# Optimization experiments

Measured on AMD Instinct MI355X. Metric: run time of the kernel, lower is better.

## Reference

```python
import jax, jax.numpy as jnp
import numpy as np

D = 128          # kg_emb_dim
H = 8            # mha_n_heads
N = 20000        # sub-graph nodes per modality
NNZ = 500000     # incidence entries per modality
E = 5000         # hyperedges per modality
C = 50           # context entities
NENT = 50000     # n_entity (rec vocab)


def hyperconv(x, theta, bias, nodes, edges, num_edges):
    # PyG-style HypergraphConv: out = D^-1 H B^-1 H^T (X Theta) + b
    xt = x @ theta                                             # [N, D]
    ones = jnp.ones(nodes.shape[0], xt.dtype)
    e_sum = jax.ops.segment_sum(xt[nodes], edges, num_segments=num_edges)   # [E, D]
    e_deg = jax.ops.segment_sum(ones, edges, num_segments=num_edges)        # [E]
    m = e_sum / jnp.maximum(e_deg, 1.0)[:, None]               # hyperedge means
    n_sum = jax.ops.segment_sum(m[edges], nodes, num_segments=x.shape[0])   # [N, D]
    n_deg = jax.ops.segment_sum(ones, nodes, num_segments=x.shape[0])       # [N]
    return n_sum / jnp.maximum(n_deg, 1.0)[:, None] + bias


def mha(q_x, kv_x, Wq, bq, Wk, bk, Wv, bv, Wo, bo):
    # torch.nn.MultiheadAttention math, batch of 1 (squeezed)
    dh = D // H
    q = (q_x @ Wq + bq).reshape(-1, H, dh)
    k = (kv_x @ Wk + bk).reshape(-1, H, dh)
    v = (kv_x @ Wv + bv).reshape(-1, H, dh)
    scores = jnp.einsum('qhd,khd->hqk', q, k) / jnp.sqrt(jnp.asarray(dh, q.dtype))
    attn = jax.nn.softmax(scores, axis=-1)
    out = jnp.einsum('hqk,khd->qhd', attn, v).reshape(-1, D)
    return out @ Wo + bo


def self_attn(h, a, b):
    # SelfAttentionBatch: softmax(tanh(h a) b) weighted sum over rows
    e = (jnp.tanh(h @ a) @ b)[:, 0]
    return jax.nn.softmax(e) @ h


def setup_inputs() -> dict:
    ks = jax.random.split(jax.random.key(0), 32)
    s = D ** (-0.5)
    inp = {
        'item_emb':   jax.random.normal(ks[0], (N, D), jnp.float32) * s,
        'entity_emb': jax.random.normal(ks[1], (N, D), jnp.float32) * s,
        'word_emb':   jax.random.normal(ks[2], (N, D), jnp.float32) * s,
        'context_entity': jax.random.normal(ks[3], (C, D), jnp.float32) * s,
        'theta_item':   jax.random.normal(ks[4], (D, D), jnp.float32) * s,
        'bias_item':    jax.random.normal(ks[5], (D,), jnp.float32) * 0.02,
        'theta_entity': jax.random.normal(ks[6], (D, D), jnp.float32) * s,
        'bias_entity':  jax.random.normal(ks[7], (D,), jnp.float32) * 0.02,
        'theta_word':   jax.random.normal(ks[8], (D, D), jnp.float32) * s,
        'bias_word':    jax.random.normal(ks[9], (D,), jnp.float32) * 0.02,
        'Wq': jax.random.normal(ks[10], (D, D), jnp.float32) * s,
        'bq': jax.random.normal(ks[11], (D,), jnp.float32) * 0.02,
        'Wk': jax.random.normal(ks[12], (D, D), jnp.float32) * s,
        'bk': jax.random.normal(ks[13], (D,), jnp.float32) * 0.02,
        'Wv': jax.random.normal(ks[14], (D, D), jnp.float32) * s,
        'bv': jax.random.normal(ks[15], (D,), jnp.float32) * 0.02,
        'Wo': jax.random.normal(ks[16], (D, D), jnp.float32) * s,
        'bo': jax.random.normal(ks[17], (D,), jnp.float32) * 0.02,
        'a_his': jax.random.normal(ks[18], (D, D), jnp.float32) * s,
        'b_his': jax.random.normal(ks[19], (D, 1), jnp.float32) * s,
        'a_kg':  jax.random.normal(ks[20], (D, D), jnp.float32) * s,
        'b_kg':  jax.random.normal(ks[21], (D, 1), jnp.float32) * s,
        'rec_W': jax.random.normal(ks[22], (D, NENT), jnp.float32) * s,
        'rec_b': jax.random.normal(ks[23], (NENT,), jnp.float32) * 0.02,
        'item_nodes':   jax.random.randint(ks[24], (NNZ,), 0, N, jnp.int32),
        'item_edges':   jax.random.randint(ks[25], (NNZ,), 0, E, jnp.int32),
        'entity_nodes': jax.random.randint(ks[26], (NNZ,), 0, N, jnp.int32),
        'entity_edges': jax.random.randint(ks[27], (NNZ,), 0, E, jnp.int32),
        'word_nodes':   jax.random.randint(ks[28], (NNZ,), 0, N, jnp.int32),
        'word_edges':   jax.random.randint(ks[29], (NNZ,), 0, E, jnp.int32),
    }
    return inp


def reference(item_emb, entity_emb, word_emb, context_entity,
              theta_item, bias_item, theta_entity, bias_entity, theta_word, bias_word,
              Wq, bq, Wk, bk, Wv, bv, Wo, bo,
              a_his, b_his, a_kg, b_kg, rec_W, rec_b,
              item_nodes, item_edges, entity_nodes, entity_edges, word_nodes, word_edges):
    ih = hyperconv(item_emb, theta_item, bias_item, item_nodes, item_edges, E)
    eh = hyperconv(entity_emb, theta_entity, bias_entity, entity_nodes, entity_edges, E)
    wh = hyperconv(word_emb, theta_word, bias_word, word_nodes, word_edges, E)
    related = jnp.concatenate([ih, eh, wh], axis=0)            # [3N, D]
    # MHItemAttention: context queries attend over related embeddings
    attentive = mha(context_entity, related, Wq, bq, Wk, bk, Wv, bv, Wo, bo)  # [C, D]
    u = self_attn(attentive, a_his, b_his)                     # [D]
    user = jnp.concatenate([context_entity, u[None]], axis=0)  # [C+1, D]
    user_repr = self_attn(user, a_kg, b_kg)                    # [D]
    scores = user_repr @ rec_W + rec_b                         # [NENT]
    return scores
```

## Files before the change

### kernel.cpp

```cpp
#include <hip/hip_runtime.h>
#include <hip/hip_bf16.h>

#define D_ 128
#define H_ 8
#define N_ 20000
#define NNZ_ 500000
#define E_ 5000
#define C_ 50
#define NENT_ 50000
#define NK_ (3*N_)
#define CAPE_ 192
#define CAPN_ 64
#define ENT_PB 4096
#define NBKT 157
#define BCAP 3648
#define ABLK 123
#define NCH3 118
#define KVBLK 235
#define BINA_B (3*ABLK)
#define NBB (3*NBKT)
#define EGB 3752

struct Ptr3f { const float* p[3]; };
struct Ptr3i { const int* p[3]; };
struct GemmB { const float* A[3]; const float* W[3]; unsigned short* C[3]; };

typedef short bf16x8 __attribute__((ext_vector_type(8)));
typedef float f32x4  __attribute__((ext_vector_type(4)));
typedef float f32x2  __attribute__((ext_vector_type(2)));

__device__ __forceinline__ unsigned short f2b(float f){
  unsigned u = __float_as_uint(f);
  u += 0x7FFFu + ((u>>16)&1u);
  return (unsigned short)(u>>16);
}
__device__ __forceinline__ unsigned pk2(float a, float b){
  return (unsigned)f2b(a) | ((unsigned)f2b(b) << 16);
}
__device__ __forceinline__ float blo(unsigned u){ return __uint_as_float(u<<16); }
__device__ __forceinline__ float bhi(unsigned u){ return __uint_as_float(u & 0xFFFF0000u); }

#define GBATCH(SRC, SREG, LBASE) { \
  uint4 uu[8]; \
  _Pragma("unroll") \
  for (int kk=0;kk<8;kk++){ \
    int idx = __shfl(SREG, (LBASE) + 4*kk + rgrp); \
    uu[kk] = *(const uint4*)((SRC) + (size_t)idx*128 + dl*8); \
  } \
  _Pragma("unroll") \
  for (int kk=0;kk<8;kk++){ \
    a01 += (f32x2){blo(uu[kk].x), bhi(uu[kk].x)}; \
    a23 += (f32x2){blo(uu[kk].y), bhi(uu[kk].y)}; \
    a45 += (f32x2){blo(uu[kk].z), bhi(uu[kk].z)}; \
    a67 += (f32x2){blo(uu[kk].w), bhi(uu[kk].w)}; \
  } }

#define PB_PACK 7500
#define PB_Z    7628
#define PB_Q    7629
#define PB_CTX  7693
#define PB_TOT  7743
__global__ __launch_bounds__(256) void prep_binA(Ptr3f xs, unsigned short* __restrict__ xb,
    const float* __restrict__ Wk, const float* __restrict__ Wv, unsigned short* __restrict__ bfB,
    unsigned short* __restrict__ mzero,
    const float* __restrict__ ctx, const float* __restrict__ Wq, const float* __restrict__ bq,
    unsigned short* __restrict__ bfQ,
    const float* __restrict__ a2, const float* __restrict__ b2, float* __restrict__ e2,
    Ptr3i nodes, Ptr3i edges,
    unsigned* __restrict__ pe_part, unsigned* __restrict__ pn_part,
    int* __restrict__ gcnt_e, int* __restrict__ gcnt_n)
{
  const int t = threadIdx.x;
  if (blockIdx.x < BINA_B){
    __shared__ unsigned lbin[ENT_PB];
    __shared__ int cnt[256], off[256];
    __shared__ int gbase[NBKT];
    __shared__ int wsum[4];
    const int mod = blockIdx.x / ABLK;
    const int xblk = blockIdx.x - mod*ABLK;
    const int* nd = nodes.p[mod];
    const int* ed = edges.p[mod];
    const int base = xblk * ENT_PB;
    const int lane = t & 63, w = t >> 6;

    int myn[16], mye[16], pos[16];
    #pragma unroll
    for (int k=0;k<16;k++){
      int i = base + t + k*256;
      if (i < NNZ_){ myn[k]=nd[i]; mye[k]=ed[i]; }
      else { myn[k]=-1; mye[k]=-1; }
    }

    cnt[t] = 0;
    __syncthreads();
    #pragma unroll
    for (int k=0;k<16;k++)
      if (mye[k] >= 0) pos[k] = atomicAdd(&cnt[mye[k]>>5], 1);
    __syncthreads();
    {
      int v = cnt[t], s = v;
      #pragma unroll
      for (int d=1; d<64; d<<=1){ int u=__shfl_up(s,d); if (lane>=d) s+=u; }
      if (lane==63) wsum[w]=s;
      __syncthreads();
      int wb=0;
      for (int i=0;i<w;i++) wb+=wsum[i];
      off[t] = wb + s - v;
      __syncthreads();
    }
    #pragma unroll
    for (int k=0;k<16;k++)
      if (mye[k] >= 0)
        lbin[off[mye[k]>>5] + pos[k]] = ((unsigned)mye[k] << 15) | (unsigned)myn[k];
    if (t < NBKT && cnt[t] > 0) gbase[t] = atomicAdd(&gcnt_e[mod*NBKT + t], cnt[t]);
    __syncthreads();
    {
      int total = off[255];
      unsigned* dstreg = pe_part + (size_t)mod*NBKT*BCAP;
      for (int i=t; i<total; i+=256){
        unsigned pk = lbin[i];
        int b = pk >> 20;
        int gp = gbase[b] + (i - off[b]);
        if (gp < BCAP) dstreg[(size_t)b*BCAP + gp] = pk;
      }
    }
    __syncthreads();

    cnt[t] = 0;
    __syncthreads();
    #pragma unroll
    for (int k=0;k<16;k++)
      if (myn[k] >= 0) pos[k] = atomicAdd(&cnt[myn[k]>>7], 1);
    __syncthreads();
    {
      int v = cnt[t], s = v;
      #pragma unroll
      for (int d=1; d<64; d<<=1){ int u=__shfl_up(s,d); if (lane>=d) s+=u; }
      if (lane==63) wsum[w]=s;
      __syncthreads();
      int wb=0;
      for (int i=0;i<w;i++) wb+=wsum[i];
      off[t] = wb + s - v;
      __syncthreads();
    }
    #pragma unroll
    for (int k=0;k<16;k++)
      if (myn[k] >= 0)
        lbin[off[myn[k]>>7] + pos[k]] = ((unsigned)myn[k] << 13) | (unsigned)mye[k];
    if (t < NBKT && cnt[t] > 0) gbase[t] = atomicAdd(&gcnt_n[mod*NBKT + t], cnt[t]);
    __syncthreads();
    {
      int total = off[255];
      unsigned* dstreg = pn_part + (size_t)mod*NBKT*BCAP;
      for (int i=t; i<total; i+=256){
        unsigned pk = lbin[i];
        int b = pk >> 20;
        int gp = gbase[b] + (i - off[b]);
        if (gp < BCAP) dstreg[(size_t)b*BCAP + gp] = pk;
      }
    }
    return;
  }

  int bid = blockIdx.x - BINA_B;
  if (bid < PB_PACK){
    int mod = bid / 2500, blk = bid - mod*2500;
    int i4 = blk*256 + t;
    float4 v = *(const float4*)(xs.p[mod] + (size_t)i4*4);
    ushort4 o; o.x=f2b(v.x); o.y=f2b(v.y); o.z=f2b(v.z); o.w=f2b(v.w);
    *(ushort4*)(xb + (size_t)mod*N_*D_ + (size_t)i4*4) = o;
  } else if (bid < PB_Z){
    int idx = (bid - PB_PACK)*256 + t;
    int j  = idx & 7;
    int L  = (idx >> 3) & 63;
    int kb = (idx >> 9) & 3;
    int tt = idx >> 11;
    int k = kb*32 + (L>>4)*8 + j;
    int x = L & 15;
    float v = (tt < 8) ? Wk[(size_t)k*128 + tt*16 + x] : Wv[(size_t)k*128 + (tt-8)*16 + x];
    bfB[idx] = f2b(v);
  } else if (bid == PB_Z){
    if (t < 64)       ((unsigned*)(xb    + (size_t)60000*128))[t]    = 0u;
    else if (t < 128) ((unsigned*)(mzero + (size_t)15000*128))[t-64] = 0u;
  } else if (bid < PB_CTX){
    int idx = (bid - PB_Q)*256 + t;
    int j  = idx & 7;
    int L  = (idx >> 3) & 63;
    int qt = (idx >> 9) & 3;
    int h  = idx >> 11;
    int k  = ((L>>4)&3)*8 + j;
    int q  = qt*16 + (L & 15);
    float val = 0.f;
    if (k < 16 && q < C_){
      const float* cr = ctx + (size_t)q*128;
      const float* wc = Wq + h*16 + k;
      float s0=0.f,s1=0.f,s2=0.f,s3=0.f;
      for (int d=0; d<128; d+=4){
        s0 = fmaf(cr[d],   wc[(size_t) d   *128], s0);
        s1 = fmaf(cr[d+1], wc[(size_t)(d+1)*128], s1);
        s2 = fmaf(cr[d+2], wc[(size_t)(d+2)*128], s2);
        s3 = fmaf(cr[d+3], wc[(size_t)(d+3)*128], s3);
      }
      val = 0.25f * (s0+s1+s2+s3 + bq[h*16+k]);
    }
    bfQ[idx] = f2b(val);
  } else {
    __shared__ float row[128];
    __shared__ float ps[128][2];
    __shared__ float red[2];
    int q = bid - PB_CTX;
    if (t < 128) row[t] = ctx[(size_t)q*128 + t];
    __syncthreads();
    int c = t & 127, half = t >> 7;
    float s = 0.f;
    int d0 = half*64;
    for (int d=d0; d<d0+64; d+=4){
      s = fmaf(row[d],   a2[(size_t) d   *128 + c], s);
      s = fmaf(row[d+1], a2[(size_t)(d+1)*128 + c], s);
      s = fmaf(row[d+2], a2[(size_t)(d+2)*128 + c], s);
      s = fmaf(row[d+3], a2[(size_t)(d+3)*128 + c], s);
    }
    ps[c][half] = s;
    __syncthreads();
    if (t < 128){
      float v = tanhf(ps[t][0] + ps[t][1]) * b2[t];
      #pragma unroll
      for (int k=32; k>=1; k>>=1) v += __shfl_xor(v, k);
      if ((t & 63) == 0) red[t>>6] = v;
    }
    __syncthreads();
    if (t == 0) e2[q] = red[0] + red[1];
  }
}

__global__ __launch_bounds__(256) void binB_e(const unsigned* __restrict__ pe_part,
    const int* __restrict__ gcnt_e, int* __restrict__ cnt_all,
    unsigned short* __restrict__ e_slot)
{
  __shared__ unsigned short ls[32*CAPE_];
  __shared__ int lc[32];
  const int mod = blockIdx.y, b = blockIdx.x, t = threadIdx.x;
  {
    unsigned short dmy = (unsigned short)(60000 - mod*20000);
    unsigned dd = (unsigned)dmy * 0x10001u;
    unsigned* lsu32 = (unsigned*)ls;
    for (int i=t; i<32*CAPE_/2; i+=256) lsu32[i] = dd;
  }
  if (t < 32) lc[t] = 0;
  __syncthreads();
  int cnt = gcnt_e[mod*NBKT + b];
  if (cnt > BCAP) cnt = BCAP;
  const unsigned* src = pe_part + ((size_t)mod*NBKT + b)*BCAP;
  for (int i=t; i<cnt; i+=256){
    unsigned pk = src[i];
    int el = (pk >> 15) - b*32;
    int n  = pk & 0x7FFF;
    int p = atomicAdd(&lc[el], 1);
    if (p < CAPE_) ls[el*CAPE_ + p] = (unsigned short)n;
  }
  __syncthreads();
  int rows = E_ - b*32; if (rows > 32) rows = 32;
  if (t < rows) cnt_all[mod*(E_+N_) + b*32 + t] = lc[t];
  const unsigned* lsu = (const unsigned*)ls;
  unsigned* dst = (unsigned*)(e_slot + ((size_t)mod*E_ + b*32)*CAPE_);
  int tot = rows*CAPE_/2;
  for (int i=t; i<tot; i+=256) dst[i] = lsu[i];
}

__global__ __launch_bounds__(256) void egather_binbn(const unsigned short* __restrict__ xb,
    const int* __restrict__ cnt_all, const unsigned short* __restrict__ e_slot,
    float* __restrict__ m_mean,
    const unsigned* __restrict__ pn_part, const int* __restrict__ gcnt_n,
    int* __restrict__ cnt_all_w, unsigned short* __restrict__ n_slot)
{
  __shared__ unsigned short ls[128*CAPN_];
  __shared__ int lc[128];
  const int t = threadIdx.x;
  if (blockIdx.x < NBB){
    const int mod = blockIdx.x / NBKT, b = blockIdx.x - mod*NBKT;
    {
      unsigned short dmy = (unsigned short)(15000 - mod*5000);
      unsigned dd = (unsigned)dmy * 0x10001u;
      unsigned* lsu32 = (unsigned*)ls;
      for (int i=t; i<128*CAPN_/2; i+=256) lsu32[i] = dd;
    }
    if (t < 128) lc[t] = 0;
    __syncthreads();
    int cnt = gcnt_n[mod*NBKT + b];
    if (cnt > BCAP) cnt = BCAP;
    const unsigned* src = pn_part + ((size_t)mod*NBKT + b)*BCAP;
    for (int i=t; i<cnt; i+=256){
      unsigned pk = src[i];
      int nl = (pk >> 13) - b*128;
      int e  = pk & 0x1FFF;
      int p = atomicAdd(&lc[nl], 1);
      if (p < CAPN_) ls[nl*CAPN_ + p] = (unsigned short)e;
    }
    __syncthreads();
    int rows = N_ - b*128; if (rows > 128) rows = 128;
    if (t < rows) cnt_all_w[mod*(E_+N_) + E_ + b*128 + t] = lc[t];
    const unsigned* lsu = (const unsigned*)ls;
    unsigned* dst = (unsigned*)(n_slot + ((size_t)mod*N_ + b*128)*CAPN_);
    int tot = rows*CAPN_/2;
    for (int i=t; i<tot; i+=256) dst[i] = lsu[i];
    return;
  }

  const int bb = blockIdx.x - NBB;
  const int x = bb & 7, k = bb >> 3;
  int mod, r;
  if (x < 6){
    mod = x / 3;
    int li = x - mod*3;
    int c = 417 - (li == 2);
    if (k < c){
      r = k*3 + li;
    } else {
      int hg = 52*x + (x >= 3) + (k - c);
      mod = 2; r = 938 + hg;
      if (r >= E_/4) return;
    }
  } else {
    mod = 2; r = k*2 + (x - 6);
  }
  const int w = t >> 6, lane = t & 63;
  const int rgrp = lane >> 4, dl = lane & 15;
  const int e = r*4 + w;
  const unsigned short* xt = xb + (size_t)mod*N_*D_;
  int cnt = cnt_all[mod*(E_+N_) + e];
  int c2 = (cnt < CAPE_) ? cnt : CAPE_;
  int c2p = (c2 + 31) & ~31;
  const unsigned short* slot = e_slot + ((size_t)mod*E_ + e)*CAPE_;
  int sv0 = slot[lane], sv1 = slot[64 + lane], sv2 = slot[128 + lane];
  f32x2 a01={0.f,0.f}, a23={0.f,0.f}, a45={0.f,0.f}, a67={0.f,0.f};

  if (c2p > 0)   GBATCH(xt, sv0, 0);
  if (c2p > 32)  GBATCH(xt, sv0, 32);
  if (c2p > 64)  GBATCH(xt, sv1, 0);
  if (c2p > 96)  GBATCH(xt, sv1, 32);
  if (c2p > 128) GBATCH(xt, sv2, 0);
  if (c2p > 160) GBATCH(xt, sv2, 32);

  float a0=a01.x, a1=a01.y, a2=a23.x, a3=a23.y, a4=a45.x, a5=a45.y, a6=a67.x, a7=a67.y;
  #pragma unroll
  for (int s=16; s<=32; s<<=1){
    a0 += __shfl_xor(a0, s); a1 += __shfl_xor(a1, s);
    a2 += __shfl_xor(a2, s); a3 += __shfl_xor(a3, s);
    a4 += __shfl_xor(a4, s); a5 += __shfl_xor(a5, s);
    a6 += __shfl_xor(a6, s); a7 += __shfl_xor(a7, s);
  }
  if (rgrp == 0){
    float inv = 1.f / fmaxf((float)cnt, 1.f);
    float* dst = m_mean + ((size_t)mod*E_ + e)*128 + dl*8;
    float4 o1; o1.x=a0*inv; o1.y=a1*inv; o1.z=a2*inv; o1.w=a3*inv;
    float4 o2; o2.x=a4*inv; o2.y=a5*inv; o2.z=a6*inv; o2.w=a7*inv;
    *(float4*)dst = o1;
    *(float4*)(dst + 4) = o2;
  }
}

__global__ __launch_bounds__(256) void gemm_b(GemmB g, int M)
{
  const float* A = g.A[blockIdx.y];
  const float* W = g.W[blockIdx.y];
  unsigned short* Cout = g.C[blockIdx.y];
  __shared__ float As[64][33];
  __shared__ float Ws[32][128];
  const int t  = threadIdx.x;
  const int br = blockIdx.x * 64;
  const int r0 = (t >> 5) * 8;
  const int c0 = (t & 31) * 4;
  const int lr = t >> 2;
  const int lk = (t & 3) * 8;
  const int wk = t >> 5;

  float acc[8][4];
  #pragma unroll
  for (int i=0;i<8;i++){ acc[i][0]=0.f; acc[i][1]=0.f; acc[i][2]=0.f; acc[i][3]=0.f; }

  for (int kb=0; kb<128; kb+=32){
    float av[8];
    const int grow = br + lr;
    if (grow < M){
      const float* p = A + (size_t)grow*128 + kb + lk;
      float4 a = ((const float4*)p)[0], b = ((const float4*)p)[1];
      av[0]=a.x;av[1]=a.y;av[2]=a.z;av[3]=a.w;av[4]=b.x;av[5]=b.y;av[6]=b.z;av[7]=b.w;
    } else {
      #pragma unroll
      for (int j=0;j<8;j++) av[j]=0.f;
    }
    float4 wv4[4];
    #pragma unroll
    for (int kk=0;kk<4;kk++) wv4[kk] = *(const float4*)&W[(size_t)(kb + wk + kk*8)*128 + c0];

    __syncthreads();
    #pragma unroll
    for (int j=0;j<8;j++) As[lr][lk+j] = av[j];
    #pragma unroll
    for (int kk=0;kk<4;kk++) *(float4*)&Ws[wk + kk*8][c0] = wv4[kk];
    __syncthreads();

    #pragma unroll
    for (int k=0;k<32;k++){
      float4 wv = *(const float4*)&Ws[k][c0];
      #pragma unroll
      for (int i=0;i<8;i++){
        float a = As[r0+i][k];
        acc[i][0] = fmaf(a, wv.x, acc[i][0]);
        acc[i][1] = fmaf(a, wv.y, acc[i][1]);
        acc[i][2] = fmaf(a, wv.z, acc[i][2]);
        acc[i][3] = fmaf(a, wv.w, acc[i][3]);
      }
    }
  }

  #pragma unroll
  for (int i=0;i<8;i++){
    int gr = br + r0 + i;
    if (gr < M){
      ushort4 o;
      o.x=f2b(acc[i][0]); o.y=f2b(acc[i][1]); o.z=f2b(acc[i][2]); o.w=f2b(acc[i][3]);
      *(ushort4*)(Cout + (size_t)gr*128 + c0) = o;
    }
  }
}

__global__ __launch_bounds__(256) void n_gather_w(const unsigned short* __restrict__ m_buf,
    const int* __restrict__ cnt_all, const unsigned short* __restrict__ n_slot,
    Ptr3f biases, unsigned short* __restrict__ relbf)
{
  int mod = blockIdx.y;
  int w = threadIdx.x >> 6, lane = threadIdx.x & 63;
  int rgrp = lane >> 4, dl = lane & 15;
  int n = blockIdx.x*4 + w;
  const unsigned short* m = m_buf + (size_t)mod*E_*D_;
  int cnt = cnt_all[mod*(E_+N_) + E_ + n];
  int c2 = (cnt < CAPN_) ? cnt : CAPN_;
  int c2p = (c2 + 31) & ~31;
  const unsigned short* slot = n_slot + ((size_t)mod*N_ + n)*CAPN_;
  int sv = slot[lane];
  f32x2 a01={0.f,0.f}, a23={0.f,0.f}, a45={0.f,0.f}, a67={0.f,0.f};
  if (c2p > 0)  GBATCH(m, sv, 0);
  if (c2p > 32) GBATCH(m, sv, 32);

  float a0=a01.x, a1=a01.y, a2=a23.x, a3=a23.y, a4=a45.x, a5=a45.y, a6=a67.x, a7=a67.y;
  #pragma unroll
  for (int s=16; s<=32; s<<=1){
    a0 += __shfl_xor(a0, s); a1 += __shfl_xor(a1, s);
    a2 += __shfl_xor(a2, s); a3 += __shfl_xor(a3, s);
    a4 += __shfl_xor(a4, s); a5 += __shfl_xor(a5, s);
    a6 += __shfl_xor(a6, s); a7 += __shfl_xor(a7, s);
  }
  if (rgrp == 0){
    float inv = 1.f / fmaxf((float)cnt, 1.f);
    const float* bs = biases.p[mod] + dl*8;
    uint4 o;
    o.x = pk2(a0*inv + bs[0], a1*inv + bs[1]);
    o.y = pk2(a2*inv + bs[2], a3*inv + bs[3]);
    o.z = pk2(a4*inv + bs[4], a5*inv + bs[5]);
    o.w = pk2(a6*inv + bs[6], a7*inv + bs[7]);
    *(uint4*)(relbf + ((size_t)mod*N_ + n)*128 + dl*8) = o;
  }
}

__global__ __launch_bounds__(256) void gemm_kv_mfma(const unsigned short* __restrict__ relbf,
    const unsigned short* __restrict__ bfB, const float* __restrict__ bk,
    const float* __restrict__ bv, unsigned short* __restrict__ Kb,
    unsigned short* __restrict__ Vtg)
{
  __shared__ unsigned short Bs[32768];
  const int t = threadIdx.x, w = t >> 6, L = t & 63;
  const int m = L & 15, quad = L >> 4, x = m;

  {
    const uint4* src = (const uint4*)bfB;
    uint4* dst = (uint4*)Bs;
    for (int i = t; i < 4096; i += 256) dst[i] = src[i];
  }
  __syncthreads();

  const int rowbase = blockIdx.x*256;
  for (int g = 0; g < 4; g++){
    const int j0 = rowbase + g*64 + w*16;

    bf16x8 a[4];
    {
      int row = j0 + m;
      int rowc = (row < NK_) ? row : (NK_-1);
      #pragma unroll
      for (int kb=0; kb<4; kb++)
        a[kb] = *(const bf16x8*)(relbf + (size_t)rowc*128 + kb*32 + quad*8);
    }

    f32x4 acc[16];
    #pragma unroll
    for (int tt=0; tt<16; tt++) acc[tt] = (f32x4){0.f,0.f,0.f,0.f};

    #pragma unroll
    for (int kb=0; kb<4; kb++){
      #pragma unroll
      for (int tt=0; tt<16; tt++){
        bf16x8 b = *(const bf16x8*)&Bs[(((tt*4 + kb)*64 + L) << 3)];
        acc[tt] = __builtin_amdgcn_mfma_f32_16x16x32_bf16(a[kb], b, acc[tt], 0, 0, 0);
      }
    }

    #pragma unroll
    for (int tt=0; tt<16; tt++){
      int h = tt & 7, kv = tt >> 3;
      float bias = (kv ? bv : bk)[h*16 + x];
      #pragma unroll
      for (int r=0; r<4; r++){
        int jr = j0 + quad*4 + r;
        if (jr < NK_){
          unsigned short val = f2b(acc[tt][r] + bias);
          if (kv == 0) Kb[(((size_t)h*NK_ + jr) << 4) + x] = val;
          else         Vtg[((size_t)(h*16 + x))*NK_ + jr] = val;
        }
      }
    }
  }
}

__global__ __launch_bounds__(256) void flash3(const unsigned short* __restrict__ Kb,
    const unsigned short* __restrict__ Vtg, const unsigned short* __restrict__ bfQ,
    float* __restrict__ part)
{
  __shared__ unsigned short P_lds[4][64][40];
  __shared__ float mbuf[4][64][18];
  const int c = blockIdx.x, h = blockIdx.y;
  const int t = threadIdx.x, w = t >> 6, L = t & 63;
  const int n = L & 15, quad = L >> 4;

  bf16x8 qb[4];
  #pragma unroll
  for (int qt=0; qt<4; qt++)
    qb[qt] = *(const bf16x8*)(bfQ + (((h*4 + qt)*64 + L) << 3));

  float Mc[4], Lc[4];
  f32x4 accq[4];
  #pragma unroll
  for (int qt=0; qt<4; qt++){ Mc[qt] = -INFINITY; Lc[qt] = 0.f; accq[qt] = (f32x4){0.f,0.f,0.f,0.f}; }

  const int base = c*512 + w*128;
  unsigned* Pw = (unsigned*)&P_lds[w][0][0];

  for (int tile=0; tile<4; tile++){
    const int j0 = base + tile*32;
    const bool dead = (j0 >= NK_);

    bf16x8 a0 = (bf16x8){0,0,0,0,0,0,0,0};
    bf16x8 a1 = a0;
    if (quad < 2){
      int k0 = j0 + n;      if (k0 > NK_-1) k0 = NK_-1;
      int k1 = j0 + 16 + n; if (k1 > NK_-1) k1 = NK_-1;
      a0 = *(const bf16x8*)(Kb + (((size_t)h*NK_ + k0) << 4) + quad*8);
      a1 = *(const bf16x8*)(Kb + (((size_t)h*NK_ + k1) << 4) + quad*8);
    }
    f32x4 s0[4], s1[4];
    #pragma unroll
    for (int qt=0; qt<4; qt++){
      s0[qt] = __builtin_amdgcn_mfma_f32_16x16x32_bf16(a0, qb[qt], (f32x4){0.f,0.f,0.f,0.f}, 0,0,0);
      s1[qt] = __builtin_amdgcn_mfma_f32_16x16x32_bf16(a1, qb[qt], (f32x4){0.f,0.f,0.f,0.f}, 0,0,0);
    }

    #pragma unroll
    for (int qt=0; qt<4; qt++){
      float mt = s0[qt][0];
      mt = fmaxf(mt, s0[qt][1]); mt = fmaxf(mt, s0[qt][2]); mt = fmaxf(mt, s0[qt][3]);
      mt = fmaxf(mt, s1[qt][0]); mt = fmaxf(mt, s1[qt][1]);
      mt = fmaxf(mt, s1[qt][2]); mt = fmaxf(mt, s1[qt][3]);
      mt = fmaxf(mt, __shfl_xor(mt, 16));
      mt = fmaxf(mt, __shfl_xor(mt, 32));
      float Mn = fmaxf(Mc[qt], mt);
      float corr = __expf(Mc[qt] - Mn);
      Mc[qt] = Mn;
      float p0[4], p1[4];
      #pragma unroll
      for (int r=0;r<4;r++){
        p0[r] = __expf(s0[qt][r] - Mn);
        p1[r] = __expf(s1[qt][r] - Mn);
      }
      if (dead){
        #pragma unroll
        for (int r=0;r<4;r++){ p0[r]=0.f; p1[r]=0.f; }
      }
      float lt = p0[0]+p0[1]+p0[2]+p0[3]+p1[0]+p1[1]+p1[2]+p1[3];
      lt += __shfl_xor(lt, 16);
      lt += __shfl_xor(lt, 32);
      Lc[qt] = Lc[qt]*corr + lt;
      int rb = (qt*16 + n)*20;
      Pw[rb + quad*2]     = pk2(p0[0], p0[1]);
      Pw[rb + quad*2 + 1] = pk2(p0[2], p0[3]);
      Pw[rb + 8 + quad*2]     = pk2(p1[0], p1[1]);
      Pw[rb + 8 + quad*2 + 1] = pk2(p1[2], p1[3]);
      #pragma unroll
      for (int r=0;r<4;r++){
        float cr = __shfl(corr, quad*4 + r);
        accq[qt][r] *= cr;
      }
    }
    __syncthreads();

    bf16x8 bv_;
    {
      int va = j0 + quad*8; if (va > NK_-8) va = NK_-8;
      bv_ = *(const bf16x8*)(Vtg + ((size_t)(h*16 + n))*NK_ + va);
    }
    #pragma unroll
    for (int qt=0; qt<4; qt++){
      bf16x8 pa = *(const bf16x8*)&P_lds[w][qt*16 + n][quad*8];
      accq[qt] = __builtin_amdgcn_mfma_f32_16x16x32_bf16(pa, bv_, accq[qt], 0,0,0);
    }
    __syncthreads();
  }

  #pragma unroll
  for (int qt=0; qt<4; qt++){
    #pragma unroll
    for (int r=0; r<4; r++)
      mbuf[w][qt*16 + quad*4 + r][2 + n] = accq[qt][r];
    if (quad == 0){
      mbuf[w][qt*16 + n][0] = Mc[qt];
      mbuf[w][qt*16 + n][1] = Lc[qt];
    }
  }
  __syncthreads();
  if (t < C_){
    float M = mbuf[0][t][0], Lm = mbuf[0][t][1];
    float A[16];
    #pragma unroll
    for (int i=0;i<16;i++) A[i] = mbuf[0][t][2+i];
    #pragma unroll
    for (int ww=1; ww<4; ww++){
      float pm = mbuf[ww][t][0], pl = mbuf[ww][t][1];
      if (pl > 0.f){
        float mn = fmaxf(M, pm);
        float c1 = __expf(M - mn), c2 = __expf(pm - mn);
        Lm = Lm*c1 + pl*c2;
        #pragma unroll
        for (int i=0;i<16;i++) A[i] = A[i]*c1 + mbuf[ww][t][2+i]*c2;
        M = mn;
      }
    }
    float* pp = part + ((size_t)(h*NCH3 + c)*C_ + t)*18;
    pp[0] = M; pp[1] = Lm;
    #pragma unroll
    for (int i=0;i<16;i++) pp[2+i] = A[i];
  }
}

__global__ __launch_bounds__(512) void merge_oproj_e1(const float* __restrict__ part,
    const float* __restrict__ Wo, const float* __restrict__ bo,
    const float* __restrict__ a1, const float* __restrict__ b1,
    float* __restrict__ attentive, float* __restrict__ e1)
{
  __shared__ float row[128];
  __shared__ float ps[128][4];
  __shared__ float orow[128];
  __shared__ float red[2];
  const int q = blockIdx.x, t = threadIdx.x;
  const int h = t >> 6, lane = t & 63;

  {
    float M = -1e30f, L = 0.f;
    float A[16];
    #pragma unroll
    for (int i=0;i<16;i++) A[i] = 0.f;

    #pragma unroll
    for (int cc=0; cc<2; cc++){
      int c = lane + cc*64;
      if (c < NCH3){
        const float* p = part + ((size_t)(h*NCH3 + c)*C_ + q)*18;
        float pm = p[0], pl = p[1];
        if (pl > 0.f){
          float Mn = fmaxf(M, pm);
          float w1 = __expf(M - Mn), w2 = __expf(pm - Mn);
          L = L*w1 + pl*w2;
          #pragma unroll
          for (int i=0;i<16;i++) A[i] = fmaf(A[i], w1, p[2+i]*w2);
          M = Mn;
        }
      }
    }
    #pragma unroll
    for (int d=32; d>=1; d>>=1){
      float pm = __shfl_xor(M, d);
      float pl = __shfl_xor(L, d);
      float Ao[16];
      #pragma unroll
      for (int i=0;i<16;i++) Ao[i] = __shfl_xor(A[i], d);
      float Mn = fmaxf(M, pm);
      float w1 = __expf(M - Mn), w2 = __expf(pm - Mn);
      L = L*w1 + pl*w2;
      #pragma unroll
      for (int i=0;i<16;i++) A[i] = fmaf(A[i], w1, Ao[i]*w2);
      M = Mn;
    }
    if (lane == 0){
      float invL = 1.f / L;
      #pragma unroll
      for (int i=0;i<16;i++) row[h*16 + i] = A[i]*invL;
    }
  }
  __syncthreads();

  const int c = t & 127, seg = t >> 7;
  {
    float s = 0.f;
    int d0 = seg*32;
    for (int d=d0; d<d0+32; d+=4){
      s = fmaf(row[d],   Wo[(size_t) d   *128 + c], s);
      s = fmaf(row[d+1], Wo[(size_t)(d+1)*128 + c], s);
      s = fmaf(row[d+2], Wo[(size_t)(d+2)*128 + c], s);
      s = fmaf(row[d+3], Wo[(size_t)(d+3)*128 + c], s);
    }
    ps[c][seg] = s;
  }
  __syncthreads();
  if (t < 128){
    float o = ps[t][0]+ps[t][1]+ps[t][2]+ps[t][3] + bo[t];
    attentive[(size_t)q*128 + t] = o;
    orow[t] = o;
  }
  __syncthreads();
  {
    float s = 0.f;
    int d0 = seg*32;
    for (int d=d0; d<d0+32; d+=4){
      s = fmaf(orow[d],   a1[(size_t) d   *128 + c], s);
      s = fmaf(orow[d+1], a1[(size_t)(d+1)*128 + c], s);
      s = fmaf(orow[d+2], a1[(size_t)(d+2)*128 + c], s);
      s = fmaf(orow[d+3], a1[(size_t)(d+3)*128 + c], s);
    }
    ps[c][seg] = s;
  }
  __syncthreads();
  if (t < 128){
    float v = tanhf(ps[t][0]+ps[t][1]+ps[t][2]+ps[t][3]) * b1[t];
    #pragma unroll
    for (int k=32; k>=1; k>>=1) v += __shfl_xor(v, k);
    if ((t & 63) == 0) red[t>>6] = v;
  }
  __syncthreads();
  if (t == 0) e1[q] = red[0] + red[1];
}

__global__ __launch_bounds__(256) void tail_scores(const float* __restrict__ attentive,
    const float* __restrict__ ctx, const float* __restrict__ a2, const float* __restrict__ b2,
    const float* __restrict__ e1, const float* __restrict__ e2,
    const float* __restrict__ recW, const float* __restrict__ recb, float* __restrict__ out)
{
  __shared__ float p[64];
  __shared__ float u[128];
  __shared__ float red[2];
  __shared__ float p2[64];
  __shared__ float ur[128];
  const int t = threadIdx.x;

  if (t == 0){
    float mx=-INFINITY;
    for (int i=0;i<C_;i++) mx=fmaxf(mx,e1[i]);
    float ss=0.f;
    for (int i=0;i<C_;i++){ p[i]=__expf(e1[i]-mx); ss+=p[i]; }
    float inv=1.f/ss;
    for (int i=0;i<C_;i++) p[i]*=inv;
  }
  __syncthreads();
  if (t < 128){
    float s=0.f;
    for (int r=0;r<C_;r++) s = fmaf(p[r], attentive[(size_t)r*128 + t], s);
    u[t] = s;
  }
  __syncthreads();
  if (t < 128){
    float s0=0.f,s1=0.f,s2=0.f,s3=0.f;
    for (int d=0; d<128; d+=4){
      s0 = fmaf(u[d],   a2[(size_t) d   *128 + t], s0);
      s1 = fmaf(u[d+1], a2[(size_t)(d+1)*128 + t], s1);
      s2 = fmaf(u[d+2], a2[(size_t)(d+2)*128 + t], s2);
      s3 = fmaf(u[d+3], a2[(size_t)(d+3)*128 + t], s3);
    }
    float v = tanhf(s0+s1+s2+s3) * b2[t];
    #pragma unroll
    for (int k=32; k>=1; k>>=1) v += __shfl_xor(v, k);
    if ((t & 63) == 0) red[t>>6] = v;
  }
  __syncthreads();
  if (t == 0){
    float elast = red[0] + red[1];
    float mx=elast;
    for (int i=0;i<C_;i++) mx=fmaxf(mx,e2[i]);
    float ss=0.f;
    for (int i=0;i<C_;i++){ p2[i]=__expf(e2[i]-mx); ss+=p2[i]; }
    float pl = __expf(elast-mx); ss += pl;
    float inv=1.f/ss;
    for (int i=0;i<C_;i++) p2[i]*=inv;
    p2[C_] = pl*inv;
  }
  __syncthreads();
  if (t < 128){
    float s=0.f;
    for (int r=0;r<C_;r++) s = fmaf(p2[r], ctx[(size_t)r*128 + t], s);
    s = fmaf(p2[C_], u[t], s);
    ur[t] = s;
  }
  __syncthreads();
  int j = blockIdx.x*256 + t;
  if (j < NENT_){
    float s0=0.f,s1=0.f,s2=0.f,s3=0.f;
    for (int d=0; d<128; d+=4){
      s0 = fmaf(ur[d],   recW[(size_t) d   *NENT_ + j], s0);
      s1 = fmaf(ur[d+1], recW[(size_t)(d+1)*NENT_ + j], s1);
      s2 = fmaf(ur[d+2], recW[(size_t)(d+2)*NENT_ + j], s2);
      s3 = fmaf(ur[d+3], recW[(size_t)(d+3)*NENT_ + j], s3);
    }
    out[j] = s0+s1+s2+s3 + recb[j];
  }
}

extern "C" void kernel_launch(void* const* d_in, const int* in_sizes, int n_in,
                              void* d_out, int out_size, void* d_ws, size_t ws_size,
                              hipStream_t stream)
{
  auto f32 = [&](int i){ return (const float*)d_in[i]; };
  Ptr3i nodes = {{(const int*)d_in[24], (const int*)d_in[26], (const int*)d_in[28]}};
  Ptr3i edges = {{(const int*)d_in[25], (const int*)d_in[27], (const int*)d_in[29]}};

  char* base = (char*)d_ws;
  int*   cnt_all = (int*)base;
  int*   gcnt_e  = (int*)(base + 300064);
  int*   gcnt_n  = gcnt_e + NBKT*3;
  unsigned short* n_slot = (unsigned short*)(base + 300064 + 4096);
  float* m_mean  = (float*)((char*)n_slot + 7680000);
  unsigned short* m_buf = (unsigned short*)((char*)m_mean + 7680000);
  unsigned short* relbf = (unsigned short*)((char*)m_buf + 3840256);
  unsigned short* bfB   = (unsigned short*)((char*)relbf + 15360000);
  unsigned short* bfQ   = (unsigned short*)((char*)bfB + 65536);
  float* attentive = (float*)((char*)bfQ + 32768);
  float* user_repr = (float*)((char*)attentive + 25600);
  float* e1buf     = user_repr + 128;
  float* e2buf     = e1buf + 64;
  float* fpart = (float*)relbf;
  char* U = (char*)(e2buf + 64);
  unsigned* pe_part = (unsigned*)U;
  unsigned* pn_part = pe_part + (size_t)3*NBKT*BCAP;
  unsigned short* e_slot = (unsigned short*)(pn_part + (size_t)3*NBKT*BCAP);
  unsigned short* xb     = e_slot + (size_t)3*E_*CAPE_;
  unsigned short* Kb  = (unsigned short*)U;
  unsigned short* Vtg = Kb + (size_t)H_*NK_*16;

  hipMemsetAsync(gcnt_e, 0, 4096, stream);

  Ptr3f xs = {{f32(0), f32(1), f32(2)}};
  prep_binA<<<BINA_B + PB_TOT, 256, 0, stream>>>(xs, xb, f32(12), f32(14), bfB, m_buf,
                                   f32(3), f32(10), f32(11), bfQ, f32(20), f32(21), e2buf,
                                   nodes, edges, pe_part, pn_part, gcnt_e, gcnt_n);

  binB_e<<<dim3(NBKT, 3), 256, 0, stream>>>(pe_part, gcnt_e, cnt_all, e_slot);

  egather_binbn<<<NBB + EGB, 256, 0, stream>>>(xb, cnt_all, e_slot, m_mean,
                                               pn_part, gcnt_n, cnt_all, n_slot);

  GemmB g;
  for (int mod=0; mod<3; mod++){
    g.A[mod] = m_mean + (size_t)mod*E_*D_;
    g.W[mod] = f32(4 + 2*mod);
    g.C[mod] = m_buf + (size_t)mod*E_*D_;
  }
  gemm_b<<<dim3((E_+63)/64, 3), 256, 0, stream>>>(g, E_);
  Ptr3f biases = {{f32(5), f32(7), f32(9)}};
  n_gather_w<<<dim3(N_/4, 3), 256, 0, stream>>>(m_buf, cnt_all, n_slot, biases, relbf);

  gemm_kv_mfma<<<KVBLK, 256, 0, stream>>>(relbf, bfB, f32(13), f32(15), Kb, Vtg);
  flash3<<<dim3(NCH3, H_), 256, 0, stream>>>(Kb, Vtg, bfQ, fpart);
  merge_oproj_e1<<<C_, 512, 0, stream>>>(fpart, f32(16), f32(17), f32(18), f32(19),
                                         attentive, e1buf);

  tail_scores<<<(NENT_+255)/256, 256, 0, stream>>>(attentive, f32(3), f32(20), f32(21),
                                                   e1buf, e2buf, f32(22), f32(23), (float*)d_out);
}
```

Measured before the change: 334.0 us.

## Stage V tiles in LDS for coalesced stores; read B from global; prescale gather offsets

The KV projection kernel no longer copies the full 64KB weight matrix into LDS. It reads the B fragments directly from global memory, where they should stay cache-resident. The transposed V output is staged in a small padded LDS tile and written back as contiguous 16-byte rows instead of scattered 2-byte stores, and bf16 conversion now uses v_cvt_pk_bf16_f32. The gather kernels prescale slot indices into byte offsets to save address arithmetic, at the cost of extra barriers per tile and global-memory B loads in the MFMA loop.

```diff
diff --git a/kernel.cpp b/kernel.cpp
--- a/kernel.cpp
+++ b/kernel.cpp
@@ -40,12 +40,12 @@
 __device__ __forceinline__ float blo(unsigned u){ return __uint_as_float(u<<16); }
 __device__ __forceinline__ float bhi(unsigned u){ return __uint_as_float(u & 0xFFFF0000u); }
 
-#define GBATCH(SRC, SREG, LBASE) { \
+#define GBATCH(SRCB, SREG, LBASE) { \
   uint4 uu[8]; \
   _Pragma("unroll") \
   for (int kk=0;kk<8;kk++){ \
-    int idx = __shfl(SREG, (LBASE) + 4*kk + rgrp); \
-    uu[kk] = *(const uint4*)((SRC) + (size_t)idx*128 + dl*8); \
+    int off = __shfl(SREG, (LBASE) + 4*kk + rgrp); \
+    uu[kk] = *(const uint4*)((SRCB) + off); \
   } \
   _Pragma("unroll") \
   for (int kk=0;kk<8;kk++){ \
@@ -326,20 +326,22 @@
   const int w = t >> 6, lane = t & 63;
   const int rgrp = lane >> 4, dl = lane & 15;
   const int e = r*4 + w;
-  const unsigned short* xt = xb + (size_t)mod*N_*D_;
+  const char* xt8 = (const char*)(xb + (size_t)mod*N_*D_) + dl*8*2;
   int cnt = cnt_all[mod*(E_+N_) + e];
   int c2 = (cnt < CAPE_) ? cnt : CAPE_;
   int c2p = (c2 + 31) & ~31;
   const unsigned short* slot = e_slot + ((size_t)mod*E_ + e)*CAPE_;
-  int sv0 = slot[lane], sv1 = slot[64 + lane], sv2 = slot[128 + lane];
+  int sv0 = ((int)slot[lane]) << 8;
+  int sv1 = ((int)slot[64 + lane]) << 8;
+  int sv2 = ((int)slot[128 + lane]) << 8;
   f32x2 a01={0.f,0.f}, a23={0.f,0.f}, a45={0.f,0.f}, a67={0.f,0.f};
 
-  if (c2p > 0)   GBATCH(xt, sv0, 0);
-  if (c2p > 32)  GBATCH(xt, sv0, 32);
-  if (c2p > 64)  GBATCH(xt, sv1, 0);
-  if (c2p > 96)  GBATCH(xt, sv1, 32);
-  if (c2p > 128) GBATCH(xt, sv2, 0);
-  if (c2p > 160) GBATCH(xt, sv2, 32);
+  if (c2p > 0)   GBATCH(xt8, sv0, 0);
+  if (c2p > 32)  GBATCH(xt8, sv0, 32);
+  if (c2p > 64)  GBATCH(xt8, sv1, 0);
+  if (c2p > 96)  GBATCH(xt8, sv1, 32);
+  if (c2p > 128) GBATCH(xt8, sv2, 0);
+  if (c2p > 160) GBATCH(xt8, sv2, 32);
 
   float a0=a01.x, a1=a01.y, a2=a23.x, a3=a23.y, a4=a45.x, a5=a45.y, a6=a67.x, a7=a67.y;
   #pragma unroll
@@ -433,15 +435,15 @@
   int w = threadIdx.x >> 6, lane = threadIdx.x & 63;
   int rgrp = lane >> 4, dl = lane & 15;
   int n = blockIdx.x*4 + w;
-  const unsigned short* m = m_buf + (size_t)mod*E_*D_;
+  const char* m8 = (const char*)(m_buf + (size_t)mod*E_*D_) + dl*8*2;
   int cnt = cnt_all[mod*(E_+N_) + E_ + n];
   int c2 = (cnt < CAPN_) ? cnt : CAPN_;
   int c2p = (c2 + 31) & ~31;
   const unsigned short* slot = n_slot + ((size_t)mod*N_ + n)*CAPN_;
-  int sv = slot[lane];
+  int sv = ((int)slot[lane]) << 8;
   f32x2 a01={0.f,0.f}, a23={0.f,0.f}, a45={0.f,0.f}, a67={0.f,0.f};
-  if (c2p > 0)  GBATCH(m, sv, 0);
-  if (c2p > 32) GBATCH(m, sv, 32);
+  if (c2p > 0)  GBATCH(m8, sv, 0);
+  if (c2p > 32) GBATCH(m8, sv, 32);
 
   float a0=a01.x, a1=a01.y, a2=a23.x, a3=a23.y, a4=a45.x, a5=a45.y, a6=a67.x, a7=a67.y;
   #pragma unroll
@@ -468,18 +470,11 @@
     const float* __restrict__ bv, unsigned short* __restrict__ Kb,
     unsigned short* __restrict__ Vtg)
 {
-  __shared__ unsigned short Bs[32768];
+  __shared__ unsigned short Vs[128][72];
   const int t = threadIdx.x, w = t >> 6, L = t & 63;
   const int m = L & 15, quad = L >> 4, x = m;
-
-  {
-    const uint4* src = (const uint4*)bfB;
-    uint4* dst = (uint4*)Bs;
-    for (int i = t; i < 4096; i += 256) dst[i] = src[i];
-  }
-  __syncthreads();
-
   const int rowbase = blockIdx.x*256;
+
   for (int g = 0; g < 4; g++){
     const int j0 = rowbase + g*64 + w*16;
 
@@ -500,25 +495,60 @@
     for (int kb=0; kb<4; kb++){
       #pragma unroll
       for (int tt=0; tt<16; tt++){
-        bf16x8 b = *(const bf16x8*)&Bs[(((tt*4 + kb)*64 + L) << 3)];
+        bf16x8 b = *(const bf16x8*)(bfB + (((tt*4 + kb)*64 + L) << 3));
         acc[tt] = __builtin_amdgcn_mfma_f32_16x16x32_bf16(a[kb], b, acc[tt], 0, 0, 0);
       }
     }
 
     #pragma unroll
-    for (int tt=0; tt<16; tt++){
-      int h = tt & 7, kv = tt >> 3;
-      float bias = (kv ? bv : bk)[h*16 + x];
-      #pragma unroll
-      for (int r=0; r<4; r++){
-        int jr = j0 + quad*4 + r;
-        if (jr < NK_){
-          unsigned short val = f2b(acc[tt][r] + bias);
-          if (kv == 0) Kb[(((size_t)h*NK_ + jr) << 4) + x] = val;
-          else         Vtg[((size_t)(h*16 + x))*NK_ + jr] = val;
-        }
-      }
-    }
+    for (int tt=0; tt<8; tt++){
+      float bias = bk[tt*16 + x];
+      unsigned p0, p1;
+      asm("v_cvt_pk_bf16_f32 %0, %1, %2" : "=v"(p0) : "v"(acc[tt][0]+bias), "v"(acc[tt][1]+bias));
+      asm("v_cvt_pk_bf16_f32 %0, %1, %2" : "=v"(p1) : "v"(acc[tt][2]+bias), "v"(acc[tt][3]+bias));
+      int jrb = j0 + quad*4;
+      if (jrb + 3 < NK_){
+        Kb[(((size_t)tt*NK_ + jrb    ) << 4) + x] = (unsigned short)p0;
+        Kb[(((size_t)tt*NK_ + jrb + 1) << 4) + x] = (unsigned short)(p0 >> 16);
+        Kb[(((size_t)tt*NK_ + jrb + 2) << 4) + x] = (unsigned short)p1;
+        Kb[(((size_t)tt*NK_ + jrb + 3) << 4) + x] = (unsigned short)(p1 >> 16);
+      } else {
+        if (jrb     < NK_) Kb[(((size_t)tt*NK_ + jrb    ) << 4) + x] = (unsigned short)p0;
+        if (jrb + 1 < NK_) Kb[(((size_t)tt*NK_ + jrb + 1) << 4) + x] = (unsigned short)(p0 >> 16);
+        if (jrb + 2 < NK_) Kb[(((size_t)tt*NK_ + jrb + 2) << 4) + x] = (unsigned short)p1;
+        if (jrb + 3 < NK_) Kb[(((size_t)tt*NK_ + jrb + 3) << 4) + x] = (unsigned short)(p1 >> 16);
+      }
+    }
+
+    #pragma unroll
+    for (int tt=8; tt<16; tt++){
+      int h = tt - 8;
+      float bias = bv[h*16 + x];
+      unsigned p0, p1;
+      asm("v_cvt_pk_bf16_f32 %0, %1, %2" : "=v"(p0) : "v"(acc[tt][0]+bias), "v"(acc[tt][1]+bias));
+      asm("v_cvt_pk_bf16_f32 %0, %1, %2" : "=v"(p1) : "v"(acc[tt][2]+bias), "v"(acc[tt][3]+bias));
+      int col = w*16 + quad*4;
+      *(unsigned*)&Vs[h*16 + x][col]     = p0;
+      *(unsigned*)&Vs[h*16 + x][col + 2] = p1;
+    }
+    __syncthreads();
+
+    {
+      int row = t >> 1, half = t & 1;
+      int c0 = half*32;
+      int jr0 = rowbase + g*64 + c0;
+      const unsigned short* src = &Vs[row][c0];
+      unsigned short* dstp = Vtg + (size_t)row*NK_ + jr0;
+      if (jr0 + 31 < NK_){
+        ((uint4*)dstp)[0] = ((const uint4*)src)[0];
+        ((uint4*)dstp)[1] = ((const uint4*)src)[1];
+        ((uint4*)dstp)[2] = ((const uint4*)src)[2];
+        ((uint4*)dstp)[3] = ((const uint4*)src)[3];
+      } else {
+        for (int c=0; c<32; c++) if (jr0 + c < NK_) dstp[c] = src[c];
+      }
+    }
+    __syncthreads();
   }
 }
 
```

Result: faster. 323.4 us (-3.2%).
